# Optimization experiments

Measured on AMD Instinct MI355X. Metric: run time of the kernel, lower is better.

The kernel has to match this reference:

```python
import jax, jax.numpy as jnp
import numpy as np

EPS = 1e-6

def _sobel_grad_mag(x):
    # x: [B, C, H, W]. Kernels are cross-correlation (as F.conv2d):
    # vertical:   out[i,j] = -x[i-1,j] + x[i+1,j]
    # horizontal: out[i,j] = -x[i,j-1] + x[i,j+1]
    # padding=1 -> zero-pad borders, same spatial output size.
    xp = jnp.pad(x, ((0, 0), (0, 0), (1, 1), (1, 1)))
    gv = xp[:, :, 2:, 1:-1] - xp[:, :, :-2, 1:-1]   # x[i+1,j] - x[i-1,j]
    gh = xp[:, :, 1:-1, 2:] - xp[:, :, 1:-1, :-2]   # x[i,j+1] - x[i,j-1]
    return jnp.sqrt(gv * gv + gh * gh + EPS)

def setup_inputs() -> dict:
    key = jax.random.key(0)
    x = jax.random.normal(key, (8, 64, 256, 256), dtype=jnp.float32)
    return {"x": x}

def reference(x):
    return _sobel_grad_mag(x)
```

## Files before the change

kernel.cpp:

```cpp
#include <hip/hip_runtime.h>
#include <math.h>


#define PLANE_H 256
#define PLANE_W 256
#define VECW 64

__global__ __launch_bounds__(256) void sobel_kernel(const float* __restrict__ x,
                                                    float* __restrict__ out,
                                                    int total_vec) {
    int idx = blockIdx.x * blockDim.x + threadIdx.x;
    if (idx >= total_vec) return;

    int j4    = idx & (VECW - 1);
    int row   = (idx >> 6) & (PLANE_H - 1);
    int plane = idx >> 14;

    size_t base = ((size_t)plane << 16) + ((size_t)row << 8) + ((size_t)j4 << 2);
    const float* p = x + base;

    float4 c  = *(const float4*)p;
    float4 up = (row > 0)           ? *(const float4*)(p - PLANE_W)
                                    : make_float4(0.f, 0.f, 0.f, 0.f);
    float4 dn = (row < PLANE_H - 1) ? *(const float4*)(p + PLANE_W)
                                    : make_float4(0.f, 0.f, 0.f, 0.f);
    float left  = (j4 > 0)        ? p[-1] : 0.f;
    float right = (j4 < VECW - 1) ? p[4]  : 0.f;

    const float eps = 1e-6f;

    float gh0 = c.y   - left;
    float gh1 = c.z   - c.x;
    float gh2 = c.w   - c.y;
    float gh3 = right - c.z;

    float gv0 = dn.x - up.x;
    float gv1 = dn.y - up.y;
    float gv2 = dn.z - up.z;
    float gv3 = dn.w - up.w;

    float4 o;
    o.x = sqrtf(gv0 * gv0 + gh0 * gh0 + eps);
    o.y = sqrtf(gv1 * gv1 + gh1 * gh1 + eps);
    o.z = sqrtf(gv2 * gv2 + gh2 * gh2 + eps);
    o.w = sqrtf(gv3 * gv3 + gh3 * gh3 + eps);

    *(float4*)(out + base) = o;
}

extern "C" void kernel_launch(void* const* d_in, const int* in_sizes, int n_in,
                              void* d_out, int out_size, void* d_ws, size_t ws_size,
                              hipStream_t stream) {
    const float* x = (const float*)d_in[0];
    float* out = (float*)d_out;
    int total_vec = out_size / 4;
    int block = 256;
    int grid = (total_vec + block - 1) / block;
    sobel_kernel<<<grid, block, 0, stream>>>(x, out, total_vec);
}
```

Before: 221.7 us.

## Compute two rows per thread, use wave shuffles for halo, nontemporal stores

Each thread now produces two adjacent output rows, loading four input rows instead of six, so vertical neighbours are reused across the pair. Left and right halo values come from cross-lane shuffles within the 64-wide wavefront instead of extra scalar loads. Outputs are written with nontemporal stores to limit cache pollution. The kernel is memory bound, so the savings come from fewer load instructions and less redundant traffic. In exchange there are half as many threads and more registers per thread.

```diff
diff --git a/kernel.cpp b/kernel.cpp
--- a/kernel.cpp
+++ b/kernel.cpp
@@ -6,46 +6,73 @@
 #define PLANE_W 256
 #define VECW 64
 
+typedef float f32x4_t __attribute__((ext_vector_type(4)));
+
+__device__ __forceinline__ void nt_store_f4(float* p, float4 v) {
+    __builtin_nontemporal_store(*(const f32x4_t*)&v, (f32x4_t*)p);
+}
+
 __global__ __launch_bounds__(256) void sobel_kernel(const float* __restrict__ x,
                                                     float* __restrict__ out,
-                                                    int total_vec) {
+                                                    int total_threads) {
     int idx = blockIdx.x * blockDim.x + threadIdx.x;
-    if (idx >= total_vec) return;
+    if (idx >= total_threads) return;
 
-    int j4    = idx & (VECW - 1);
-    int row   = (idx >> 6) & (PLANE_H - 1);
-    int plane = idx >> 14;
+    int lane  = idx & (VECW - 1);
+    int rp    = (idx >> 6) & 127;
+    int plane = idx >> 13;
+    int r     = rp << 1;
 
-    size_t base = ((size_t)plane << 16) + ((size_t)row << 8) + ((size_t)j4 << 2);
+    size_t base = ((size_t)plane << 16) + ((size_t)r << 8) + ((size_t)lane << 2);
     const float* p = x + base;
 
-    float4 c  = *(const float4*)p;
-    float4 up = (row > 0)           ? *(const float4*)(p - PLANE_W)
-                                    : make_float4(0.f, 0.f, 0.f, 0.f);
-    float4 dn = (row < PLANE_H - 1) ? *(const float4*)(p + PLANE_W)
-                                    : make_float4(0.f, 0.f, 0.f, 0.f);
-    float left  = (j4 > 0)        ? p[-1] : 0.f;
-    float right = (j4 < VECW - 1) ? p[4]  : 0.f;
+    const float4 zero = make_float4(0.f, 0.f, 0.f, 0.f);
+
+    float4 b = *(const float4*)p;
+    float4 c = *(const float4*)(p + PLANE_W);
+    float4 a = (r > 0)             ? *(const float4*)(p - PLANE_W)     : zero;
+    float4 d = (r < PLANE_H - 2)   ? *(const float4*)(p + 2 * PLANE_W) : zero;
+
+    float bl = __shfl_up(b.w, 1);   bl = (lane == 0)        ? 0.f : bl;
+    float br = __shfl_down(b.x, 1); br = (lane == VECW - 1) ? 0.f : br;
+    float cl = __shfl_up(c.w, 1);   cl = (lane == 0)        ? 0.f : cl;
+    float cr = __shfl_down(c.x, 1); cr = (lane == VECW - 1) ? 0.f : cr;
 
     const float eps = 1e-6f;
 
-    float gh0 = c.y   - left;
-    float gh1 = c.z   - c.x;
-    float gh2 = c.w   - c.y;
-    float gh3 = right - c.z;
+    {
+        float gh0 = b.y - bl;
+        float gh1 = b.z - b.x;
+        float gh2 = b.w - b.y;
+        float gh3 = br  - b.z;
+        float gv0 = c.x - a.x;
+        float gv1 = c.y - a.y;
+        float gv2 = c.z - a.z;
+        float gv3 = c.w - a.w;
+        float4 o;
+        o.x = sqrtf(gv0 * gv0 + gh0 * gh0 + eps);
+        o.y = sqrtf(gv1 * gv1 + gh1 * gh1 + eps);
+        o.z = sqrtf(gv2 * gv2 + gh2 * gh2 + eps);
+        o.w = sqrtf(gv3 * gv3 + gh3 * gh3 + eps);
+        nt_store_f4(out + base, o);
+    }
 
-    float gv0 = dn.x - up.x;
-    float gv1 = dn.y - up.y;
-    float gv2 = dn.z - up.z;
-    float gv3 = dn.w - up.w;
-
-    float4 o;
-    o.x = sqrtf(gv0 * gv0 + gh0 * gh0 + eps);
-    o.y = sqrtf(gv1 * gv1 + gh1 * gh1 + eps);
-    o.z = sqrtf(gv2 * gv2 + gh2 * gh2 + eps);
-    o.w = sqrtf(gv3 * gv3 + gh3 * gh3 + eps);
-
-    *(float4*)(out + base) = o;
+    {
+        float gh0 = c.y - cl;
+        float gh1 = c.z - c.x;
+        float gh2 = c.w - c.y;
+        float gh3 = cr  - c.z;
+        float gv0 = d.x - b.x;
+        float gv1 = d.y - b.y;
+        float gv2 = d.z - b.z;
+        float gv3 = d.w - b.w;
+        float4 o;
+        o.x = sqrtf(gv0 * gv0 + gh0 * gh0 + eps);
+        o.y = sqrtf(gv1 * gv1 + gh1 * gh1 + eps);
+        o.z = sqrtf(gv2 * gv2 + gh2 * gh2 + eps);
+        o.w = sqrtf(gv3 * gv3 + gh3 * gh3 + eps);
+        nt_store_f4(out + base + PLANE_W, o);
+    }
 }
 
 extern "C" void kernel_launch(void* const* d_in, const int* in_sizes, int n_in,
@@ -53,8 +80,8 @@
                               hipStream_t stream) {
     const float* x = (const float*)d_in[0];
     float* out = (float*)d_out;
-    int total_vec = out_size / 4;
+    int total_threads = out_size / 8;
     int block = 256;
-    int grid = (total_vec + block - 1) / block;
-    sobel_kernel<<<grid, block, 0, stream>>>(x, out, total_vec);
+    int grid = (total_threads + block - 1) / block;
+    sobel_kernel<<<grid, block, 0, stream>>>(x, out, total_threads);
 }
```

After: 222.9 us. About the same (+0.5%).
